# Kernel optimization log

Measured on AMD Instinct MI355X. Metric: run time of the kernel, lower is better.

Reference implementation:

```python
import jax, jax.numpy as jnp
import numpy as np

N_RAYS = 65536   # 256x256 image
T_SAMPLES = 128  # StratifiedRayStepSampler default
HID = 16         # tiny radiance-field MLP hidden width


def setup_inputs() -> dict:
    key = jax.random.key(0)
    ks = jax.random.split(key, 8)
    o = jax.random.normal(ks[0], (N_RAYS, 3), jnp.float32)
    d = jax.random.normal(ks[1], (N_RAYS, 3), jnp.float32)
    tnear = jnp.zeros((N_RAYS, 1), jnp.float32)
    # tfar in [1,5): guarantees tfar > tnear for every ray
    tfar = 1.0 + 4.0 * jax.random.uniform(ks[2], (N_RAYS, 1), jnp.float32)
    noise = jax.random.uniform(ks[3], (T_SAMPLES, N_RAYS, 1), jnp.float32)
    W1 = jax.random.normal(ks[4], (3, HID), jnp.float32) * 0.5
    b1 = jnp.zeros((HID,), jnp.float32)
    w_sigma = jax.random.normal(ks[5], (HID, 1), jnp.float32) * 0.5
    W_rgb = jax.random.normal(ks[6], (HID, 3), jnp.float32) * 0.5
    return {"o": o, "d": d, "tnear": tnear, "tfar": tfar, "noise": noise,
            "W1": W1, "b1": b1, "w_sigma": w_sigma, "W_rgb": W_rgb}


def reference(o, d, tnear, tfar, noise, W1, b1, w_sigma, W_rgb):
    T = noise.shape[0]
    dnorm = jnp.linalg.norm(d, axis=-1, keepdims=True)            # (N,1)
    # stratified sampling: ts[i] = tnear + (tfar-tnear)*(i+u_i)/T  -> (T,N,1)
    bins = (jnp.arange(T, dtype=o.dtype)[:, None, None] + noise) / T
    ts = tnear[None] + (tfar - tnear)[None] * bins                # (T,N,1)
    # evaluate rays and query radiance field
    xyz = o[None] + ts * d[None]                                  # (T,N,3)
    h = jax.nn.relu(xyz @ W1 + b1)                                # (T,N,HID)
    sigma = jax.nn.softplus(h @ w_sigma)                          # (T,N,1) density
    rgb = jax.nn.sigmoid(h @ W_rgb)                               # (T,N,3) color
    # volumetric integration along sample axis
    delta = jnp.concatenate([ts[1:] - ts[:-1], tfar[None] - ts[-1:]], axis=0)
    sd = sigma * delta * dnorm[None]                              # (T,N,1)
    # exclusive cumsum -> log-transmittance (stable cumprod)
    log_trans = jnp.concatenate(
        [jnp.zeros_like(sd[:1]), -jnp.cumsum(sd[:-1], axis=0)], axis=0)
    weights = jnp.exp(log_trans) * (1.0 - jnp.exp(-sd))           # (T,N,1)
    color = jnp.sum(weights * rgb, axis=0)                        # (N,3)
    depth = jnp.sum(weights * ts, axis=0)                         # (N,1)
    alpha = jnp.sum(weights, axis=0)                              # (N,1)
    return jnp.concatenate([color, depth, alpha], axis=-1)        # (N,5)
```

## Files before the change

### kernel.cpp

```cpp
#include <hip/hip_runtime.h>
#include <math.h>

#define N_RAYS 65536
#define T_SAMPLES 128
#define HID 16

#define RAYS_PER_BLOCK 64
#define CHUNKS 4
#define CHUNK_LEN (T_SAMPLES / CHUNKS)

#define L2E 1.4426950408889634f

__global__ __launch_bounds__(256, 4) void radiance_kernel(
    const float* __restrict__ o,
    const float* __restrict__ d,
    const float* __restrict__ tnear,
    const float* __restrict__ tfar,
    const float* __restrict__ noise,
    const float* __restrict__ W1,
    const float* __restrict__ b1,
    const float* __restrict__ w_sigma,
    const float* __restrict__ W_rgb,
    float* __restrict__ out)
{
    const int lane  = threadIdx.x & 63;
    const int chunk = threadIdx.x >> 6;
    const int ray   = blockIdx.x * RAYS_PER_BLOCK + lane;

    const float ox = o[ray*3+0], oy = o[ray*3+1], oz = o[ray*3+2];
    const float dx = d[ray*3+0], dy = d[ray*3+1], dz = d[ray*3+2];
    const float tn = tnear[ray];
    const float tf = tfar[ray];
    const float dnorm = sqrtf(dx*dx + dy*dy + dz*dz);
    const float sc = (tf - tn) * (1.0f / (float)T_SAMPLES);

    float A[HID], B[HID];
#pragma unroll
    for (int j = 0; j < HID; ++j) {
        const float w0 = W1[0*HID + j], w1 = W1[1*HID + j], w2 = W1[2*HID + j];
        A[j] = fmaf(ox, w0, fmaf(oy, w1, fmaf(oz, w2, b1[j])));
        B[j] = fmaf(dx, w0, fmaf(dy, w1, dz * w2));
    }
    float WS[HID], WR[HID], WG[HID], WB[HID];
#pragma unroll
    for (int j = 0; j < HID; ++j) {
        WS[j] = w_sigma[j];
        WR[j] = W_rgb[j*3+0];
        WG[j] = W_rgb[j*3+1];
        WB[j] = W_rgb[j*3+2];
    }

    const int t0 = chunk * CHUNK_LEN;
    const float nz0 = noise[(size_t)t0 * N_RAYS + ray];
    float fi = (float)t0;
    float ts = fmaf(sc, fi + nz0, tn);

    float lt = 1.0f;
    float cr = 0.f, cg = 0.f, cb = 0.f, cd = 0.f, ca = 0.f;

    for (int i = 0; i < CHUNK_LEN; ++i) {
        const int t = t0 + i;
        const bool has_next = (t + 1 < T_SAMPLES);
        float nz_next = 0.0f;
        if (has_next) nz_next = noise[(size_t)(t+1) * N_RAYS + ray];

        float sp = 0.f, rr = 0.f, gg = 0.f, bb = 0.f;
#pragma unroll
        for (int j = 0; j < HID; ++j) {
            const float h = fmaxf(fmaf(ts, B[j], A[j]), 0.0f);
            sp = fmaf(h, WS[j], sp);
            rr = fmaf(h, WR[j], rr);
            gg = fmaf(h, WG[j], gg);
            bb = fmaf(h, WB[j], bb);
        }

        const float ts_next = has_next ? fmaf(sc, fi + 1.0f + nz_next, tn) : tf;

        const float e  = __builtin_amdgcn_exp2f(-fabsf(sp) * L2E);
        const float l2 = fmaf(fmaxf(sp, 0.0f), L2E, __builtin_amdgcn_logf(1.0f + e));
        const float dd = (ts_next - ts) * dnorm;
        const float et = __builtin_amdgcn_exp2f(-dd * l2);

        const float r = __builtin_amdgcn_rcpf(1.0f + __builtin_amdgcn_exp2f(-rr * L2E));
        const float g = __builtin_amdgcn_rcpf(1.0f + __builtin_amdgcn_exp2f(-gg * L2E));
        const float b = __builtin_amdgcn_rcpf(1.0f + __builtin_amdgcn_exp2f(-bb * L2E));

        const float w = lt * (1.0f - et);
        cr = fmaf(w, r, cr);
        cg = fmaf(w, g, cg);
        cb = fmaf(w, b, cb);
        cd = fmaf(w, ts, cd);
        ca += w;
        lt *= et;
        ts = ts_next;
        fi += 1.0f;
    }

    __shared__ float s_lt[CHUNKS][RAYS_PER_BLOCK];
    __shared__ float s_acc[CHUNKS][5][RAYS_PER_BLOCK];
    s_lt[chunk][lane] = lt;
    s_acc[chunk][0][lane] = cr;
    s_acc[chunk][1][lane] = cg;
    s_acc[chunk][2][lane] = cb;
    s_acc[chunk][3][lane] = cd;
    s_acc[chunk][4][lane] = ca;
    __syncthreads();

    if (chunk == 0) {
        float scale = 1.0f;
        float a0 = 0.f, a1 = 0.f, a2 = 0.f, a3 = 0.f, a4 = 0.f;
#pragma unroll
        for (int c = 0; c < CHUNKS; ++c) {
            a0 = fmaf(scale, s_acc[c][0][lane], a0);
            a1 = fmaf(scale, s_acc[c][1][lane], a1);
            a2 = fmaf(scale, s_acc[c][2][lane], a2);
            a3 = fmaf(scale, s_acc[c][3][lane], a3);
            a4 = fmaf(scale, s_acc[c][4][lane], a4);
            scale *= s_lt[c][lane];
        }
        out[ray*5+0] = a0;
        out[ray*5+1] = a1;
        out[ray*5+2] = a2;
        out[ray*5+3] = a3;
        out[ray*5+4] = a4;
    }
}

extern "C" void kernel_launch(void* const* d_in, const int* in_sizes, int n_in,
                              void* d_out, int out_size, void* d_ws, size_t ws_size,
                              hipStream_t stream) {
    const float* o       = (const float*)d_in[0];
    const float* d       = (const float*)d_in[1];
    const float* tnear   = (const float*)d_in[2];
    const float* tfar    = (const float*)d_in[3];
    const float* noise   = (const float*)d_in[4];
    const float* W1      = (const float*)d_in[5];
    const float* b1      = (const float*)d_in[6];
    const float* w_sigma = (const float*)d_in[7];
    const float* W_rgb   = (const float*)d_in[8];
    float* out = (float*)d_out;

    dim3 block(64 * CHUNKS);
    dim3 grid(N_RAYS / RAYS_PER_BLOCK);
    hipLaunchKernelGGL(radiance_kernel, grid, block, 0, stream,
                       o, d, tnear, tfar, noise, W1, b1, w_sigma, W_rgb, out);
}
```

Measured before the change: 113.6 us.

## Prefetch noise rows ahead in registers and fold dnorm into sample parameter

Noise values are prefetched PF=4 steps ahead into a register ring buffer, so global load latency overlaps with the MLP math instead of stalling each iteration. The sample coordinate is rescaled by the ray-direction norm (Bp = B/dnorm, u = t*dnorm), which removes the per-step multiply by dnorm in the delta computation. Depth is divided back by dnorm at the end. This costs extra registers and may slightly change rounding.

```diff
diff --git a/kernel.cpp b/kernel.cpp
--- a/kernel.cpp
+++ b/kernel.cpp
@@ -8,6 +8,7 @@
 #define RAYS_PER_BLOCK 64
 #define CHUNKS 4
 #define CHUNK_LEN (T_SAMPLES / CHUNKS)
+#define PF 4
 
 #define L2E 1.4426950408889634f
 
@@ -27,19 +28,33 @@
     const int chunk = threadIdx.x >> 6;
     const int ray   = blockIdx.x * RAYS_PER_BLOCK + lane;
 
+    const int t0 = chunk * CHUNK_LEN;
+    const float* __restrict__ nrow = noise + ray;
+
+    const float nz0 = nrow[(size_t)t0 * N_RAYS];
+    float nzbuf[PF];
+#pragma unroll
+    for (int k = 0; k < PF; ++k)
+        nzbuf[k] = nrow[(size_t)(t0 + 1 + k) * N_RAYS];
+
     const float ox = o[ray*3+0], oy = o[ray*3+1], oz = o[ray*3+2];
     const float dx = d[ray*3+0], dy = d[ray*3+1], dz = d[ray*3+2];
     const float tn = tnear[ray];
     const float tf = tfar[ray];
     const float dnorm = sqrtf(dx*dx + dy*dy + dz*dz);
-    const float sc = (tf - tn) * (1.0f / (float)T_SAMPLES);
+    const float rdn   = 1.0f / dnorm;
+    const float sc    = (tf - tn) * (1.0f / (float)T_SAMPLES);
 
-    float A[HID], B[HID];
+    const float scd = sc * dnorm;
+    const float tnd = tn * dnorm;
+    const float uf  = tf * dnorm;
+
+    float A[HID], Bp[HID];
 #pragma unroll
     for (int j = 0; j < HID; ++j) {
         const float w0 = W1[0*HID + j], w1 = W1[1*HID + j], w2 = W1[2*HID + j];
-        A[j] = fmaf(ox, w0, fmaf(oy, w1, fmaf(oz, w2, b1[j])));
-        B[j] = fmaf(dx, w0, fmaf(dy, w1, dz * w2));
+        A[j]  = fmaf(ox, w0, fmaf(oy, w1, fmaf(oz, w2, b1[j])));
+        Bp[j] = fmaf(dx, w0, fmaf(dy, w1, dz * w2)) * rdn;
     }
     float WS[HID], WR[HID], WG[HID], WB[HID];
 #pragma unroll
@@ -50,50 +65,54 @@
         WB[j] = W_rgb[j*3+2];
     }
 
-    const int t0 = chunk * CHUNK_LEN;
-    const float nz0 = noise[(size_t)t0 * N_RAYS + ray];
-    float fi = (float)t0;
-    float ts = fmaf(sc, fi + nz0, tn);
+    float u    = fmaf(scd, (float)t0 + nz0, tnd);
+    float base = fmaf(scd, (float)(t0 + 1), tnd);
 
     float lt = 1.0f;
     float cr = 0.f, cg = 0.f, cb = 0.f, cd = 0.f, ca = 0.f;
 
-    for (int i = 0; i < CHUNK_LEN; ++i) {
-        const int t = t0 + i;
-        const bool has_next = (t + 1 < T_SAMPLES);
-        float nz_next = 0.0f;
-        if (has_next) nz_next = noise[(size_t)(t+1) * N_RAYS + ray];
+    for (int ii = 0; ii < CHUNK_LEN; ii += PF) {
+#pragma unroll
+        for (int k = 0; k < PF; ++k) {
+            const int t = t0 + ii + k;
 
-        float sp = 0.f, rr = 0.f, gg = 0.f, bb = 0.f;
+            float u_next = fmaf(scd, nzbuf[k], base);
+            if (t == T_SAMPLES - 1) u_next = uf;
+            base += scd;
+
+            int rrow = t + 1 + PF;
+            if (rrow > T_SAMPLES - 1) rrow = T_SAMPLES - 1;
+            nzbuf[k] = nrow[(size_t)rrow * N_RAYS];
+
+            float sp = 0.f, rr = 0.f, gg = 0.f, bb = 0.f;
 #pragma unroll
-        for (int j = 0; j < HID; ++j) {
-            const float h = fmaxf(fmaf(ts, B[j], A[j]), 0.0f);
-            sp = fmaf(h, WS[j], sp);
-            rr = fmaf(h, WR[j], rr);
-            gg = fmaf(h, WG[j], gg);
-            bb = fmaf(h, WB[j], bb);
+            for (int j = 0; j < HID; ++j) {
+                const float h = fmaxf(fmaf(u, Bp[j], A[j]), 0.0f);
+                sp = fmaf(h, WS[j], sp);
+                rr = fmaf(h, WR[j], rr);
+                gg = fmaf(h, WG[j], gg);
+                bb = fmaf(h, WB[j], bb);
+            }
+
+            const float e  = __builtin_amdgcn_exp2f(-fabsf(sp) * L2E);
+            const float l2 = fmaf(fmaxf(sp, 0.0f), L2E,
+                                  __builtin_amdgcn_logf(1.0f + e));
+            const float dd = u_next - u;
+            const float et = __builtin_amdgcn_exp2f(-dd * l2);
+
+            const float r = __builtin_amdgcn_rcpf(1.0f + __builtin_amdgcn_exp2f(-rr * L2E));
+            const float g = __builtin_amdgcn_rcpf(1.0f + __builtin_amdgcn_exp2f(-gg * L2E));
+            const float b = __builtin_amdgcn_rcpf(1.0f + __builtin_amdgcn_exp2f(-bb * L2E));
+
+            const float w = fmaf(-et, lt, lt);
+            cr = fmaf(w, r, cr);
+            cg = fmaf(w, g, cg);
+            cb = fmaf(w, b, cb);
+            cd = fmaf(w, u, cd);
+            ca += w;
+            lt *= et;
+            u = u_next;
         }
-
-        const float ts_next = has_next ? fmaf(sc, fi + 1.0f + nz_next, tn) : tf;
-
-        const float e  = __builtin_amdgcn_exp2f(-fabsf(sp) * L2E);
-        const float l2 = fmaf(fmaxf(sp, 0.0f), L2E, __builtin_amdgcn_logf(1.0f + e));
-        const float dd = (ts_next - ts) * dnorm;
-        const float et = __builtin_amdgcn_exp2f(-dd * l2);
-
-        const float r = __builtin_amdgcn_rcpf(1.0f + __builtin_amdgcn_exp2f(-rr * L2E));
-        const float g = __builtin_amdgcn_rcpf(1.0f + __builtin_amdgcn_exp2f(-gg * L2E));
-        const float b = __builtin_amdgcn_rcpf(1.0f + __builtin_amdgcn_exp2f(-bb * L2E));
-
-        const float w = lt * (1.0f - et);
-        cr = fmaf(w, r, cr);
-        cg = fmaf(w, g, cg);
-        cb = fmaf(w, b, cb);
-        cd = fmaf(w, ts, cd);
-        ca += w;
-        lt *= et;
-        ts = ts_next;
-        fi += 1.0f;
     }
 
     __shared__ float s_lt[CHUNKS][RAYS_PER_BLOCK];
@@ -121,7 +140,7 @@
         out[ray*5+0] = a0;
         out[ray*5+1] = a1;
         out[ray*5+2] = a2;
-        out[ray*5+3] = a3;
+        out[ray*5+3] = a3 * rdn;
         out[ray*5+4] = a4;
     }
 }
```

Result: no change. 113.8 us (+0.1%).
